# Optimization experiments

Measured on AMD Instinct MI355X. Metric: run time of the kernel, lower is better.

Reference implementation:

```python
import jax, jax.numpy as jnp
import numpy as np

B, S, D, NH = 2, 2048, 2048, 16
HD = D // NH  # 128


def setup_inputs() -> dict:
    key = jax.random.key(0)
    ks = jax.random.split(key, 7)
    s = 1.0 / np.sqrt(D)
    return {
        "hidden_states": jax.random.normal(ks[0], (B, S, D), dtype=jnp.float32),
        "Wq": jax.random.normal(ks[1], (D, D), dtype=jnp.float32) * s,
        "Wk": jax.random.normal(ks[2], (D, D), dtype=jnp.float32) * s,
        "Wv": jax.random.normal(ks[3], (D, D), dtype=jnp.float32) * s,
        "Wo": jax.random.normal(ks[4], (D, D), dtype=jnp.float32) * s,
        # phase projections: hidden -> num_heads (zero-init in the module; use small
        # random values so the phase path is numerically exercised)
        "Wpq": jax.random.normal(ks[5], (D, NH), dtype=jnp.float32) * 0.02,
        "Wpk": jax.random.normal(ks[6], (D, NH), dtype=jnp.float32) * 0.02,
    }


def reference(hidden_states, Wq, Wk, Wv, Wo, Wpq, Wpk):
    x = hidden_states  # [B,S,D]
    # ---- base_attn: standard causal multi-head self-attention ----
    q = (x @ Wq).reshape(B, S, NH, HD).transpose(0, 2, 1, 3)  # [B,H,S,hd]
    k = (x @ Wk).reshape(B, S, NH, HD).transpose(0, 2, 1, 3)
    v = (x @ Wv).reshape(B, S, NH, HD).transpose(0, 2, 1, 3)
    scores = jnp.einsum("bhqd,bhkd->bhqk", q, k) / np.sqrt(HD)  # [B,H,S,S]
    causal = jnp.tril(jnp.ones((S, S), dtype=bool))
    scores = jnp.where(causal, scores, jnp.float32(-1e9))
    probs = jax.nn.softmax(scores, axis=-1)
    ctx = jnp.einsum("bhqk,bhkd->bhqd", probs, v)  # [B,H,S,hd]
    attn_output = ctx.transpose(0, 2, 1, 3).reshape(B, S, D) @ Wo  # [B,S,D]
    # ---- phase modulation ----
    # original: cos(pq[b,q,None,h] - pk[b,None,k,h]).mean(dims=(k,h))  -> [B,S]
    # identity: cos(a-b) = cos a * cos b + sin a * sin b lets us avoid the
    # [B,S,S,H] tensor; the math is identical.
    pq = x @ Wpq  # [B,S,H]
    pk = x @ Wpk  # [B,S,H]
    Ck = jnp.cos(pk).sum(axis=1)  # [B,H]
    Sk = jnp.sin(pk).sum(axis=1)  # [B,H]
    phase_mod = (jnp.cos(pq) * Ck[:, None, :] + jnp.sin(pq) * Sk[:, None, :]).sum(-1) / (S * NH)  # [B,S]
    return attn_output * (1.0 + 0.1 * phase_mod[..., None])
```

## Files before the change

kernel.cpp:

```cpp
#include <hip/hip_runtime.h>
#include <hip/hip_bf16.h>

typedef __attribute__((ext_vector_type(8))) short short8;
typedef __attribute__((ext_vector_type(4))) float f32x4;
typedef __attribute__((ext_vector_type(16))) float f32x16;
typedef __attribute__((ext_vector_type(4))) int i32x4;
typedef unsigned short u16;

#define S_LEN 2048
#define D_DIM 2048
#define NHEAD 16
#define HDIM 128
#define M_ROWS 4096

#define MFMA(a,b,c) __builtin_amdgcn_mfma_f32_16x16x32_bf16(a,b,c,0,0,0)
#define MFMA32(a,b,c) __builtin_amdgcn_mfma_f32_32x32x16_bf16(a,b,c,0,0,0)

__device__ __forceinline__ u16 f2bf(float f) {
  union { float f; unsigned u; } v; v.f = f;
  unsigned r = v.u + 0x7fffu + ((v.u >> 16) & 1u);
  return (u16)(r >> 16);
}

__device__ __forceinline__ void async16(void* lds, const void* g) {
  __builtin_amdgcn_global_load_lds(
      (const __attribute__((address_space(1))) unsigned*)g,
      (__attribute__((address_space(3))) unsigned*)lds, 16, 0, 0);
}

__device__ __forceinline__ unsigned cvtpk(float lo, float hi) {
  unsigned r;
  asm("v_cvt_pk_bf16_f32 %0, %1, %2" : "=v"(r) : "v"(lo), "v"(hi));
  return r;
}
__device__ __forceinline__ void plswap(unsigned& x, unsigned& y) {
  asm("v_permlane32_swap_b32 %0, %1" : "+v"(x), "+v"(y));
}

__global__ void k_cvt_x(const float* __restrict__ x, u16* __restrict__ xb) {
  int i = blockIdx.x * 256 + threadIdx.x;
  float4 v = reinterpret_cast<const float4*>(x)[i];
  ushort4 o;
  o.x = f2bf(v.x); o.y = f2bf(v.y); o.z = f2bf(v.z); o.w = f2bf(v.w);
  reinterpret_cast<ushort4*>(xb)[i] = o;
}

__global__ void k_cvt_wt(const float* __restrict__ W, u16* __restrict__ Wt) {
  __shared__ u16 tile[32][33];
  int n0 = blockIdx.x * 32, k0 = blockIdx.y * 32;
  int tx = threadIdx.x & 31, ty = threadIdx.x >> 5;
#pragma unroll
  for (int i = 0; i < 4; i++)
    tile[ty + i * 8][tx] = f2bf(W[(size_t)(k0 + ty + i * 8) * D_DIM + n0 + tx]);
  __syncthreads();
#pragma unroll
  for (int i = 0; i < 4; i++)
    Wt[(size_t)(n0 + ty + i * 8) * D_DIM + k0 + tx] = tile[tx][ty + i * 8];
}

__global__ void k_vtrans(const u16* __restrict__ V, u16* __restrict__ Vt) {
  __shared__ u16 tile[32][33];
  int s0 = blockIdx.x * 32, d0 = blockIdx.y * 32, bh = blockIdx.z;
  const u16* Vp = V + (size_t)bh * S_LEN * HDIM;
  u16* Vtp = Vt + (size_t)bh * HDIM * S_LEN;
  int tx = threadIdx.x & 31, ty = threadIdx.x >> 5;
#pragma unroll
  for (int i = 0; i < 4; i++)
    tile[ty + i * 8][tx] = Vp[(size_t)(s0 + ty + i * 8) * HDIM + d0 + tx];
  __syncthreads();
#pragma unroll
  for (int i = 0; i < 4; i++)
    Vtp[(size_t)(d0 + ty + i * 8) * S_LEN + s0 + tx] = tile[tx][ty + i * 8];
}

template <int MODE>
__global__ __launch_bounds__(512, 1) void k_gemm8p(const u16* __restrict__ A,
                                                   const u16* __restrict__ Bt,
                                                   void* __restrict__ outp,
                                                   const float* __restrict__ fac) {
  constexpr int BUFSZ = 49152;
  __shared__ __align__(16) char lds[2 * BUFSZ];
  const int m0 = blockIdx.y * 128, n0 = blockIdx.x * 256;
  const int t = threadIdx.x;
  const int w = t >> 6, l = t & 63;
  const int wr = (w >> 2) * 64, wc = (w & 3) * 64;
  const int lr = l & 15, lq = l >> 4;
  const char* Ab = (const char*)A;
  const char* Bb = (const char*)Bt;

  f32x4 acc[4][4] = {};

  const int sub = w >> 2, ww = w & 3;
  const int abase = (ww & 1) * 16 + (ww >> 1) * 64;
  const int bbase = (w >> 1) * 64 + (w & 1) * 16;
  const int rr = l >> 2, sl = l & 3;

  auto stageA = [&](int tt, int nb, int mh) {
    const int base = abase + mh * 32;
    const int row = base + rr;
    async16(lds + nb * BUFSZ + sub * 8192 + base * 64,
            Ab + (size_t)(m0 + row) * 4096 + tt * 128 + sub * 64 +
                ((sl ^ ((row >> 1) & 3)) * 16));
  };
  auto stageB = [&](int tt, int nb, int nh) {
    const int base = bbase + nh * 32;
    const int row = base + rr;
#pragma unroll
    for (int j = 0; j < 2; j++)
      async16(lds + nb * BUFSZ + 16384 + j * 16384 + base * 64,
              Bb + (size_t)(n0 + row) * 4096 + tt * 128 + j * 64 +
                  ((sl ^ ((row >> 1) & 3)) * 16));
  };

  auto readA = [&](short8 af[2][2], int buf, int mh) {
#pragma unroll
    for (int mi = 0; mi < 2; mi++)
#pragma unroll
      for (int ks = 0; ks < 2; ks++) {
        const int row = wr + mh * 32 + mi * 16 + lr;
        af[mi][ks] = *reinterpret_cast<const short8*>(
            lds + buf * BUFSZ + ks * 8192 + row * 64 +
            ((lq ^ ((row >> 1) & 3)) * 16));
      }
  };
  auto readB = [&](short8 bf[2][2], int buf, int nh) {
#pragma unroll
    for (int ni = 0; ni < 2; ni++)
#pragma unroll
      for (int ks = 0; ks < 2; ks++) {
        const int row = wc + nh * 32 + ni * 16 + lr;
        bf[ni][ks] = *reinterpret_cast<const short8*>(
            lds + buf * BUFSZ + 16384 + ks * 16384 + row * 64 +
            ((lq ^ ((row >> 1) & 3)) * 16));
      }
  };

#define QUAD(AF, BF, MH, NH)                                                \
  {                                                                         \
    __builtin_amdgcn_s_setprio(1);                                          \
    _Pragma("unroll") for (int mi = 0; mi < 2; mi++)                        \
    _Pragma("unroll") for (int ni = 0; ni < 2; ni++)                        \
    _Pragma("unroll") for (int ks = 0; ks < 2; ks++)                        \
      acc[(MH)*2 + mi][(NH)*2 + ni] =                                       \
          MFMA(AF[mi][ks], BF[ni][ks], acc[(MH)*2 + mi][(NH)*2 + ni]);      \
    __builtin_amdgcn_s_setprio(0);                                          \
  }
#define VMW(N) asm volatile("s_waitcnt vmcnt(" #N ")" ::: "memory")
#define BAR()                         \
  do {                                \
    __builtin_amdgcn_s_barrier();     \
    asm volatile("" ::: "memory");    \
  } while (0)

  stageA(0, 0, 0); stageB(0, 0, 0);
  stageA(0, 0, 1);
  stageB(0, 0, 1);

  short8 af0[2][2], af1[2][2], bfr[2][2];
  const int NT = D_DIM / 64;
  for (int tt = 0; tt < NT; tt++) {
    const int buf = tt & 1, nb = buf ^ 1;
    const bool pf = (tt + 1 < NT);
    VMW(3); BAR();
    if (pf) { stageA(tt + 1, nb, 0); stageB(tt + 1, nb, 0); }
    readA(af0, buf, 0); readB(bfr, buf, 0);
    QUAD(af0, bfr, 0, 0);
    if (pf) VMW(5); else VMW(2);
    BAR();
    if (pf) stageA(tt + 1, nb, 1);
    readA(af1, buf, 1);
    QUAD(af1, bfr, 1, 0);
    if (pf) VMW(4); else VMW(0);
    BAR();
    if (pf) stageB(tt + 1, nb, 1);
    readB(bfr, buf, 1);
    QUAD(af1, bfr, 1, 1);
    BAR();
    QUAD(af0, bfr, 0, 1);
  }
#undef QUAD
#undef VMW
#undef BAR

#pragma unroll
  for (int gm = 0; gm < 4; gm++) {
#pragma unroll
    for (int gn = 0; gn < 4; gn++) {
#pragma unroll
      for (int r = 0; r < 4; r++) {
        const int row = m0 + wr + gm * 16 + lq * 4 + r;
        const int col = n0 + wc + gn * 16 + lr;
        const float v = acc[gm][gn][r];
        if (MODE == 0) {
          const int mat = col >> 11;
          const int hh = (col >> 7) & 15;
          ((u16*)outp)[(size_t)mat * 8388608 +
                       (((size_t)((row >> 11) * NHEAD + hh)) * S_LEN + (row & 2047)) * HDIM +
                       (col & 127)] = f2bf(v);
        } else {
          ((float*)outp)[(size_t)row * D_DIM + col] = v * (1.0f + 0.1f * fac[row]);
        }
      }
    }
  }
}

__global__ __launch_bounds__(256) void k_phase_proj(const u16* __restrict__ xb,
                                                    const float* __restrict__ Wpq,
                                                    const float* __restrict__ Wpk,
                                                    float* __restrict__ pq,
                                                    float* __restrict__ pk) {
  __shared__ u16 xs[16][136];
  __shared__ float2 ws[128][16];
  const int t = threadIdx.x;
  const int m0 = blockIdx.x * 16;
  const int h = t & 15, r = t >> 4;
  float sq = 0.f, sk = 0.f;
  for (int kc = 0; kc < D_DIM; kc += 128) {
    *reinterpret_cast<short8*>(&xs[t >> 4][(t & 15) * 8]) =
        *reinterpret_cast<const short8*>(
            &xb[(size_t)(m0 + (t >> 4)) * D_DIM + kc + (t & 15) * 8]);
#pragma unroll
    for (int j = 0; j < 8; j++) {
      const int idx = j * 256 + t;
      const int k = idx >> 4, hh = idx & 15;
      ws[k][hh] = make_float2(Wpq[(size_t)(kc + k) * NHEAD + hh],
                              Wpk[(size_t)(kc + k) * NHEAD + hh]);
    }
    __syncthreads();
#pragma unroll
    for (int k8 = 0; k8 < 16; k8++) {
      const short8 x8 = *reinterpret_cast<const short8*>(&xs[r][k8 * 8]);
#pragma unroll
      for (int j = 0; j < 8; j++) {
        union { float f; unsigned u; } c;
        c.u = ((unsigned)(u16)x8[j]) << 16;
        const float2 wv = ws[k8 * 8 + j][h];
        sq += c.f * wv.x;
        sk += c.f * wv.y;
      }
    }
    __syncthreads();
  }
  pq[(size_t)(m0 + r) * NHEAD + h] = sq;
  pk[(size_t)(m0 + r) * NHEAD + h] = sk;
}

__device__ __forceinline__ float wave_sum(float v) {
  v += __shfl_xor(v, 1);  v += __shfl_xor(v, 2);  v += __shfl_xor(v, 4);
  v += __shfl_xor(v, 8);  v += __shfl_xor(v, 16); v += __shfl_xor(v, 32);
  return v;
}

__global__ void k_phase_ck(const float* __restrict__ pk, float* __restrict__ Ck,
                           float* __restrict__ Sk) {
  int bh = blockIdx.x, b = bh >> 4, h = bh & 15;
  float c = 0.f, s = 0.f;
  for (int ss = threadIdx.x; ss < S_LEN; ss += 256) {
    float v = pk[((size_t)b * S_LEN + ss) * NHEAD + h];
    c += cosf(v); s += sinf(v);
  }
  c = wave_sum(c); s = wave_sum(s);
  __shared__ float rc[4], rs[4];
  int wv = threadIdx.x >> 6;
  if ((threadIdx.x & 63) == 0) { rc[wv] = c; rs[wv] = s; }
  __syncthreads();
  if (threadIdx.x == 0) {
    Ck[bh] = rc[0] + rc[1] + rc[2] + rc[3];
    Sk[bh] = rs[0] + rs[1] + rs[2] + rs[3];
  }
}

__global__ void k_phase_mod(const float* __restrict__ pq, const float* __restrict__ Ck,
                            const float* __restrict__ Sk, float* __restrict__ pm) {
  int m = blockIdx.x * 256 + threadIdx.x;
  int b = m >> 11;
  float a = 0.f;
#pragma unroll
  for (int h = 0; h < NHEAD; h++) {
    float v = pq[(size_t)m * NHEAD + h];
    a += cosf(v) * Ck[b * NHEAD + h] + sinf(v) * Sk[b * NHEAD + h];
  }
  pm[m] = a * (1.0f / (S_LEN * NHEAD));
}

__global__ __launch_bounds__(256, 2) void k_attn(const u16* __restrict__ Q,
                                                 const u16* __restrict__ K,
                                                 const u16* __restrict__ Vt,
                                                 u16* __restrict__ ctx) {
  const int bh = blockIdx.x;
  const int gy = blockIdx.y;
  const int g = (gy < 8) ? (15 - gy) : (gy - 8);
  const int b = bh >> 4, h = bh & 15;
  const int t = threadIdx.x;
  const int w = t >> 6, l = t & 63;
  const int ln = l & 31, hi = l >> 5;
  const int q0w = g * 128 + w * 32;
  const int qq = q0w + ln;
  const float scale = 0.08838834764831845f;

  const u16* Qp = Q + (size_t)bh * S_LEN * HDIM;
  const char* Kg = (const char*)(K + (size_t)bh * S_LEN * HDIM);
  const char* Vg = (const char*)(Vt + (size_t)bh * HDIM * S_LEN);

  __shared__ __align__(16) char Ks[2][16384];
  __shared__ __align__(16) char Vs[2][16384];

  auto stage = [&](int t64, int buf) {
    const int k0 = t64 * 64;
#pragma unroll
    for (int i = 0; i < 4; i++) {
      const int key = i * 16 + w * 4 + (l >> 4);
      async16(Ks[buf] + i * 4096 + w * 1024,
              Kg + (size_t)(k0 + key) * 256 + (((l & 15) * 16) ^ ((key & 15) << 4)));
      const int d = i * 32 + w * 8 + (l >> 3);
      async16(Vs[buf] + i * 4096 + w * 1024,
              Vg + (size_t)d * (S_LEN * 2) + k0 * 2 + (((l & 7) * 16) ^ ((d & 7) << 4)));
    }
  };

  short8 qf[8];
#pragma unroll
  for (int c = 0; c < 8; c++)
    qf[c] = *reinterpret_cast<const short8*>(Qp + (size_t)qq * HDIM + c * 16 + hi * 8);

  f32x16 o[4];
#pragma unroll
  for (int ds = 0; ds < 4; ds++)
#pragma unroll
    for (int r = 0; r < 16; r++) o[ds][r] = 0.f;
  float mrun = -1e30f, lsum = 0.f;

  const int nt = (g + 1) * 2;
  stage(0, 0);
  for (int t64 = 0; t64 < nt; t64++) {
    const int buf = t64 & 1;
    const int k0 = t64 * 64;
    asm volatile("s_waitcnt vmcnt(0)" ::: "memory");
    __syncthreads();
    if (t64 + 1 < nt) stage(t64 + 1, buf ^ 1);
    if (k0 < q0w + 32) {
      f32x16 s[2];
#pragma unroll
      for (int ks = 0; ks < 2; ks++)
#pragma unroll
        for (int r = 0; r < 16; r++) s[ks][r] = 0.f;
      __builtin_amdgcn_s_setprio(1);
#pragma unroll
      for (int ks = 0; ks < 2; ks++) {
        const int key = ks * 32 + ln;
        const char* kb = Ks[buf] + key * 256;
        const unsigned swzk = (unsigned)((key & 15) << 4);
#pragma unroll
        for (int c = 0; c < 8; c++) {
          const short8 kf = *reinterpret_cast<const short8*>(
              kb + (((unsigned)(c * 32 + hi * 16)) ^ swzk));
          s[ks] = MFMA32(kf, qf[c], s[ks]);
        }
      }
      __builtin_amdgcn_s_setprio(0);
      float p[32];
      float mx = -1e30f;
#pragma unroll
      for (int ks = 0; ks < 2; ks++)
#pragma unroll
        for (int r = 0; r < 16; r++) {
          const int key = k0 + ks * 32 + (r & 3) + 8 * (r >> 2) + 4 * hi;
          const float v = (key <= qq) ? s[ks][r] * scale : -1e30f;
          p[ks * 16 + r] = v;
          mx = fmaxf(mx, v);
        }
      mx = fmaxf(mx, __shfl_xor(mx, 32));
      const float nm = fmaxf(mrun, mx);
      const float f = __expf(mrun - nm);
      float rs = 0.f;
#pragma unroll
      for (int i = 0; i < 32; i++) { p[i] = __expf(p[i] - nm); rs += p[i]; }
      rs += __shfl_xor(rs, 32);
      lsum = lsum * f + rs;
      mrun = nm;
#pragma unroll
      for (int ds = 0; ds < 4; ds++)
#pragma unroll
        for (int r = 0; r < 16; r++) o[ds][r] *= f;
      short8 bfr[4];
#pragma unroll
      for (int sub = 0; sub < 2; sub++) {
#pragma unroll
        for (int half = 0; half < 2; half++) {
          const int pb = sub * 16 + half * 8;
          unsigned X1 = cvtpk(p[pb + 0], p[pb + 1]);
          unsigned X2 = cvtpk(p[pb + 2], p[pb + 3]);
          unsigned Y1 = cvtpk(p[pb + 4], p[pb + 5]);
          unsigned Y2 = cvtpk(p[pb + 6], p[pb + 7]);
          plswap(X1, Y1);
          plswap(X2, Y2);
          i32x4 bw;
          bw[0] = (int)X1; bw[1] = (int)X2; bw[2] = (int)Y1; bw[3] = (int)Y2;
          bfr[sub * 2 + half] = __builtin_bit_cast(short8, bw);
        }
      }
      __builtin_amdgcn_s_setprio(1);
#pragma unroll
      for (int ds = 0; ds < 4; ds++) {
        const int d = ds * 32 + ln;
        const char* vb = Vs[buf] + d * 128;
        const unsigned swzv = (unsigned)((d & 7) << 4);
#pragma unroll
        for (int slot = 0; slot < 4; slot++) {
          const short8 vf = *reinterpret_cast<const short8*>(
              vb + (((unsigned)(slot * 32 + hi * 16)) ^ swzv));
          o[ds] = MFMA32(vf, bfr[slot], o[ds]);
        }
      }
      __builtin_amdgcn_s_setprio(0);
    }
  }

  const float rl = 1.0f / lsum;
#pragma unroll
  for (int ds = 0; ds < 4; ds++) {
#pragma unroll
    for (int rq = 0; rq < 4; rq++) {
      const int d = ds * 32 + 8 * rq + 4 * hi;
      ushort4 pk4;
      pk4.x = f2bf(o[ds][rq * 4 + 0] * rl);
      pk4.y = f2bf(o[ds][rq * 4 + 1] * rl);
      pk4.z = f2bf(o[ds][rq * 4 + 2] * rl);
      pk4.w = f2bf(o[ds][rq * 4 + 3] * rl);
      *reinterpret_cast<ushort4*>(ctx + ((size_t)(b * S_LEN + qq)) * D_DIM + h * HDIM + d) = pk4;
    }
  }
}

extern "C" void kernel_launch(void* const* d_in, const int* in_sizes, int n_in,
                              void* d_out, int out_size, void* d_ws, size_t ws_size,
                              hipStream_t stream) {
  const float* x   = (const float*)d_in[0];
  const float* Wq  = (const float*)d_in[1];
  const float* Wk  = (const float*)d_in[2];
  const float* Wv  = (const float*)d_in[3];
  const float* Wo  = (const float*)d_in[4];
  const float* Wpq = (const float*)d_in[5];
  const float* Wpk = (const float*)d_in[6];

  char* ws = (char*)d_ws;
  u16* xb   = (u16*)(ws + 0);
  u16* Wqt  = (u16*)(ws + 16777216);
  u16* Wkt  = (u16*)(ws + 25165824);
  u16* Wvt  = (u16*)(ws + 33554432);
  u16* Wot  = (u16*)(ws + 41943040);
  u16* Qb   = (u16*)(ws + 50331648);
  u16* Kb   = (u16*)(ws + 67108864);
  u16* Vb   = (u16*)(ws + 83886080);
  u16* Vt   = (u16*)(ws + 100663296);
  float* pq = (float*)(ws + 117440512);
  float* pk = (float*)(ws + 117702656);
  float* Ck = (float*)(ws + 117964800);
  float* Sk = (float*)(ws + 117964928);
  float* pm = (float*)(ws + 117965056);

  k_cvt_x<<<dim3(M_ROWS * D_DIM / 1024), 256, 0, stream>>>(x, xb);
  k_cvt_wt<<<dim3(64, 64), 256, 0, stream>>>(Wq, Wqt);
  k_cvt_wt<<<dim3(64, 64), 256, 0, stream>>>(Wk, Wkt);
  k_cvt_wt<<<dim3(64, 64), 256, 0, stream>>>(Wv, Wvt);
  k_cvt_wt<<<dim3(64, 64), 256, 0, stream>>>(Wo, Wot);

  k_gemm8p<0><<<dim3(24, 32), 512, 0, stream>>>(xb, Wqt, Qb, nullptr);

  k_vtrans<<<dim3(64, 4, 32), 256, 0, stream>>>(Vb, Vt);

  k_phase_proj<<<dim3(256), 256, 0, stream>>>(xb, Wpq, Wpk, pq, pk);
  k_phase_ck<<<dim3(32), 256, 0, stream>>>(pk, Ck, Sk);
  k_phase_mod<<<dim3(16), 256, 0, stream>>>(pq, Ck, Sk, pm);

  k_attn<<<dim3(32, 16), 256, 0, stream>>>(Qb, Kb, Vt, Vb );

  k_gemm8p<1><<<dim3(8, 32), 512, 0, stream>>>(Vb , Wot, (void*)d_out, pm);
}
```

Before: 335.8 us.

## Triple-buffer GEMM LDS pipeline and merge weight conversions into one launch

Moves the GEMM main loop from double to triple buffering: LDS grows to three 48KB stages and tiles are prefetched two iterations ahead, with the vmcnt waits retuned to match. This lets more global loads stay in flight and hides memory latency better. In exchange the kernel uses 144KB of LDS and the waitcnt bookkeeping becomes more fragile. Separately, the four weight transpose/convert launches are merged into one launch over a z-dimension to save launch overhead.

```diff
diff --git a/kernel.cpp b/kernel.cpp
--- a/kernel.cpp
+++ b/kernel.cpp
@@ -45,8 +45,14 @@
   reinterpret_cast<ushort4*>(xb)[i] = o;
 }
 
-__global__ void k_cvt_wt(const float* __restrict__ W, u16* __restrict__ Wt) {
+__global__ void k_cvt_wt4(const float* __restrict__ W0, const float* __restrict__ W1,
+                          const float* __restrict__ W2, const float* __restrict__ W3,
+                          u16* __restrict__ T0, u16* __restrict__ T1,
+                          u16* __restrict__ T2, u16* __restrict__ T3) {
   __shared__ u16 tile[32][33];
+  const int z = blockIdx.z;
+  const float* W = (z == 0) ? W0 : (z == 1) ? W1 : (z == 2) ? W2 : W3;
+  u16* Wt = (z == 0) ? T0 : (z == 1) ? T1 : (z == 2) ? T2 : T3;
   int n0 = blockIdx.x * 32, k0 = blockIdx.y * 32;
   int tx = threadIdx.x & 31, ty = threadIdx.x >> 5;
 #pragma unroll
@@ -74,12 +80,12 @@
 }
 
 template <int MODE>
-__global__ __launch_bounds__(512, 1) void k_gemm8p(const u16* __restrict__ A,
-                                                   const u16* __restrict__ Bt,
-                                                   void* __restrict__ outp,
-                                                   const float* __restrict__ fac) {
+__device__ __forceinline__ void gemm_body(const u16* __restrict__ A,
+                                          const u16* __restrict__ Bt,
+                                          void* __restrict__ outp,
+                                          const float* __restrict__ fac,
+                                          char* lds) {
   constexpr int BUFSZ = 49152;
-  __shared__ __align__(16) char lds[2 * BUFSZ];
   const int m0 = blockIdx.y * 128, n0 = blockIdx.x * 256;
   const int t = threadIdx.x;
   const int w = t >> 6, l = t & 63;
@@ -155,24 +161,29 @@
   stageA(0, 0, 0); stageB(0, 0, 0);
   stageA(0, 0, 1);
   stageB(0, 0, 1);
+  stageA(1, 1, 0); stageB(1, 1, 0);
+  stageA(1, 1, 1);
+  stageB(1, 1, 1);
 
   short8 af0[2][2], af1[2][2], bfr[2][2];
   const int NT = D_DIM / 64;
   for (int tt = 0; tt < NT; tt++) {
-    const int buf = tt & 1, nb = buf ^ 1;
-    const bool pf = (tt + 1 < NT);
-    VMW(3); BAR();
-    if (pf) { stageA(tt + 1, nb, 0); stageB(tt + 1, nb, 0); }
+    const int buf = tt % 3;
+    const int sb = (tt + 2) % 3;
+    const bool pf2 = (tt + 2 < NT);
+    if (tt < NT - 1) VMW(9); else VMW(3);
+    BAR();
+    if (pf2) { stageA(tt + 2, sb, 0); stageB(tt + 2, sb, 0); }
     readA(af0, buf, 0); readB(bfr, buf, 0);
     QUAD(af0, bfr, 0, 0);
-    if (pf) VMW(5); else VMW(2);
+    if (tt < NT - 2) VMW(11); else if (tt == NT - 2) VMW(8); else VMW(2);
     BAR();
-    if (pf) stageA(tt + 1, nb, 1);
+    if (pf2) stageA(tt + 2, sb, 1);
     readA(af1, buf, 1);
     QUAD(af1, bfr, 1, 0);
-    if (pf) VMW(4); else VMW(0);
+    if (tt < NT - 2) VMW(10); else if (tt == NT - 2) VMW(6); else VMW(0);
     BAR();
-    if (pf) stageB(tt + 1, nb, 1);
+    if (pf2) stageB(tt + 2, sb, 1);
     readB(bfr, buf, 1);
     QUAD(af1, bfr, 1, 1);
     BAR();
@@ -203,6 +214,21 @@
       }
     }
   }
+}
+
+__global__ __launch_bounds__(512, 1) void k_qkv(const u16* __restrict__ A,
+                                                const u16* __restrict__ Bt,
+                                                void* __restrict__ outp) {
+  __shared__ __align__(16) char lds[3 * 49152];
+  gemm_body<0>(A, Bt, outp, nullptr, lds);
+}
+
+__global__ __launch_bounds__(512, 1) void k_oproj(const u16* __restrict__ A,
+                                                  const u16* __restrict__ Bt,
+                                                  void* __restrict__ outp,
+                                                  const float* __restrict__ fac) {
+  __shared__ __align__(16) char lds[3 * 49152];
+  gemm_body<1>(A, Bt, outp, fac, lds);
 }
 
 __global__ __launch_bounds__(256) void k_phase_proj(const u16* __restrict__ xb,
@@ -461,12 +487,9 @@
   float* pm = (float*)(ws + 117965056);
 
   k_cvt_x<<<dim3(M_ROWS * D_DIM / 1024), 256, 0, stream>>>(x, xb);
-  k_cvt_wt<<<dim3(64, 64), 256, 0, stream>>>(Wq, Wqt);
-  k_cvt_wt<<<dim3(64, 64), 256, 0, stream>>>(Wk, Wkt);
-  k_cvt_wt<<<dim3(64, 64), 256, 0, stream>>>(Wv, Wvt);
-  k_cvt_wt<<<dim3(64, 64), 256, 0, stream>>>(Wo, Wot);
-
-  k_gemm8p<0><<<dim3(24, 32), 512, 0, stream>>>(xb, Wqt, Qb, nullptr);
+  k_cvt_wt4<<<dim3(64, 64, 4), 256, 0, stream>>>(Wq, Wk, Wv, Wo, Wqt, Wkt, Wvt, Wot);
+
+  k_qkv<<<dim3(24, 32), 512, 0, stream>>>(xb, Wqt, Qb);
 
   k_vtrans<<<dim3(64, 4, 32), 256, 0, stream>>>(Vb, Vt);
 
@@ -476,5 +499,5 @@
 
   k_attn<<<dim3(32, 16), 256, 0, stream>>>(Qb, Kb, Vt, Vb );
 
-  k_gemm8p<1><<<dim3(8, 32), 512, 0, stream>>>(Vb , Wot, (void*)d_out, pm);
-}
+  k_oproj<<<dim3(8, 32), 512, 0, stream>>>(Vb , Wot, (void*)d_out, pm);
+}
```

Result: no change. 331.4 us (-1.3%).
